# Kernel optimization log

Measured on AMD Instinct MI355X. Metric: run time of the kernel, lower is better.

Reference implementation:

```python
import jax, jax.numpy as jnp
import numpy as np

RATES = (6, 12, 18, 24)  # dilation/padding per branch


def _offset_conv(x, w, b, rate):
    # mmcv ConvModule with norm_cfg=None: conv (bias=True) + ReLU
    y = jax.lax.conv_general_dilated(
        x, w, window_strides=(1, 1),
        padding=[(rate, rate), (rate, rate)],
        rhs_dilation=(rate, rate),
        dimension_numbers=('NCHW', 'OIHW', 'NCHW'))
    return jax.nn.relu(y + b[None, :, None, None])


def _deform_conv(x, offset, w, rate):
    # DCNv1: 3x3 deformable conv, stride 1, padding=dilation=rate,
    # deformable_groups=1, no bias. Zero padding outside image (bilinear).
    B, C, H, W = x.shape
    K = 9  # 3x3 kernel taps, row-major; offset channels [2k]=dy, [2k+1]=dx
    ky = (jnp.arange(K) // 3 - 1).astype(x.dtype)
    kx = (jnp.arange(K) % 3 - 1).astype(x.dtype)
    off = offset.reshape(B, K, 2, H, W)
    gy = jnp.arange(H, dtype=x.dtype)
    gx = jnp.arange(W, dtype=x.dtype)
    # sampling coords [B,K,H,W]: p0 + dilated kernel offset + learned offset
    py = gy[None, None, :, None] + ky[None, :, None, None] * rate + off[:, :, 0]
    px = gx[None, None, None, :] + kx[None, :, None, None] * rate + off[:, :, 1]
    y0 = jnp.floor(py)
    x0 = jnp.floor(px)
    wy = (py - y0)[:, None]  # [B,1,K,H,W]
    wx = (px - x0)[:, None]
    y0i = y0.astype(jnp.int32)
    x0i = x0.astype(jnp.int32)
    xf = x.reshape(B, C, H * W)

    def gather(yi, xi):
        valid = (yi >= 0) & (yi < H) & (xi >= 0) & (xi < W)
        idx = (jnp.clip(yi, 0, H - 1) * W + jnp.clip(xi, 0, W - 1)).reshape(B, K * H * W)
        v = jnp.take_along_axis(xf, idx[:, None, :], axis=2).reshape(B, C, K, H, W)
        return v * valid[:, None].astype(x.dtype)

    samp = (gather(y0i, x0i) * (1 - wy) * (1 - wx)
            + gather(y0i, x0i + 1) * (1 - wy) * wx
            + gather(y0i + 1, x0i) * wy * (1 - wx)
            + gather(y0i + 1, x0i + 1) * wy * wx)  # [B,C,K,H,W]
    return jnp.einsum('oik,bikhw->bohw', w.reshape(w.shape[0], C, K), samp)


def setup_inputs() -> dict:
    key = jax.random.key(0)
    k1, k2, k3 = jax.random.split(key, 3)
    B, C, H, W = 2, 256, 64, 64
    Cout, R = 256, len(RATES)
    x = jax.random.normal(k1, (B, C, H, W), dtype=jnp.float32)
    dweights = jax.random.normal(k2, (R, Cout, C, 3, 3), dtype=jnp.float32) * 0.02
    oweights = jax.random.normal(k3, (R, 18, C, 3, 3), dtype=jnp.float32) * 0.01
    obias = jnp.zeros((R, 18), dtype=jnp.float32)
    return {"x": x, "dweights": dweights, "oweights": oweights, "obias": obias}


def reference(x, dweights, oweights, obias):
    R = len(RATES)
    outs = []
    for i in range(R):
        j = (i - 1) % R  # source quirk: offsets[i-1] (wraps to last for i=0)
        off = _offset_conv(x, oweights[j], obias[j], RATES[j])
        outs.append(_deform_conv(x, off, dweights[i], RATES[i]))
    return jnp.concatenate(outs, axis=1)
```

## Files before the change

### kernel.cpp

```cpp
#include <hip/hip_runtime.h>
#include <hip/hip_bf16.h>

typedef __attribute__((ext_vector_type(4))) float f32x4;
typedef __attribute__((ext_vector_type(2))) _Float16 h2;
typedef __attribute__((ext_vector_type(8))) _Float16 f16x8;

#define LGKM_BARRIER() asm volatile("s_waitcnt lgkmcnt(0)\n\ts_barrier" ::: "memory")

__global__ __launch_bounds__(256) void transpose_x_hwc_f16(const float* __restrict__ x,
                                                           unsigned short* __restrict__ x16h) {
    __shared__ float s[64][65];
    int blk = blockIdx.x;
    int b = blk >> 8, ct = (blk >> 6) & 3, pt = blk & 63;
    int c0 = ct * 64, p0 = pt * 64;
    int tid = threadIdx.x;
    int tr = tid >> 6, tc = tid & 63;
#pragma unroll
    for (int i = 0; i < 16; ++i) {
        int c = i * 4 + tr;
        s[c][tc] = x[((size_t)b * 256 + c0 + c) * 4096 + p0 + tc];
    }
    __syncthreads();
#pragma unroll
    for (int i = 0; i < 16; ++i) {
        int pp = i * 4 + tr;
        _Float16 h = (_Float16)s[tc][pp];
        x16h[((size_t)b * 4096 + p0 + pp) * 256 + c0 + tc] = *(unsigned short*)&h;
    }
}

__global__ __launch_bounds__(256) void transpose_dw_f16(const float* __restrict__ dw,
                                                        unsigned short* __restrict__ wTh) {
    int idx = blockIdx.x * 256 + threadIdx.x;
    int c = idx & 255;
    int o = (idx >> 8) & 255;
    int rest = idx >> 16;
    int k = rest % 9, i = rest / 9;
    _Float16 h = (_Float16)dw[(((i << 8) + o) * 256 + c) * 9 + k];
    wTh[idx] = *(unsigned short*)&h;
}

__global__ __launch_bounds__(256) void transpose_ow_f16(const float* __restrict__ ow,
                                                        unsigned short* __restrict__ owTh) {
    int idx = blockIdx.x * 256 + threadIdx.x;
    int c = idx & 255;
    int m = (idx >> 8) & 31;
    int rk = idx >> 13;
    int k = rk % 9, r = rk / 9;
    float v = (m < 18) ? ow[((r * 18 + m) * 256 + c) * 9 + k] : 0.f;
    _Float16 h = (_Float16)v;
    owTh[idx] = *(unsigned short*)&h;
}

__global__ __launch_bounds__(512) void offset_mfma2f(const unsigned short* __restrict__ x16h,
                                                     const unsigned short* __restrict__ owTh,
                                                     const float* __restrict__ obias,
                                                     float* __restrict__ off) {
    __shared__ short    s_a[4][32][8];
    __shared__ short    s_b[4][128][8];
    __shared__ int      s_pix[9][128];
    __shared__ unsigned s_msk[9][128];

    const int blk = blockIdx.x;
    const int r = (blk & 7) >> 1, b = blk & 1;
    const int px0 = (blk >> 3) << 7;
    const int rate = 6 * (r + 1);

    const int tid = threadIdx.x;
    const int lane = tid & 63;
    const int w = tid >> 6;
    const int kg = lane >> 4, lm = lane & 15;
    const int sg = tid >> 7, spx = tid & 127;
    const int mA = (tid & 127) >> 2, kgA = tid & 3;

    const unsigned short* xbh = x16h + (size_t)b * 1048576;
    const unsigned short* wrb = owTh + (size_t)r * 9 * 32 * 256;

    for (int e = tid; e < 1152; e += 512) {
        int k = e >> 7, pl = e & 127;
        int pg = px0 + pl;
        int yy = (pg >> 6) + (k / 3 - 1) * rate;
        int xx = (pg & 63) + (k % 3 - 1) * rate;
        bool v = ((unsigned)yy < 64u) && ((unsigned)xx < 64u);
        int cy = min(max(yy, 0), 63), cx = min(max(xx, 0), 63);
        s_pix[k][pl] = cy * 64 + cx;
        s_msk[k][pl] = v ? 0xFFFFFFFFu : 0u;
    }
    __syncthreads();

    f32x4 acc0 = (f32x4)(0.f), acc1 = (f32x4)(0.f);

    uint4 a, v;
    if (tid < 128) a = *(const uint4*)(wrb + (size_t)mA * 256 + kgA * 8);
    {
        int pix = s_pix[0][spx];
        v = *(const uint4*)(xbh + (size_t)pix * 256 + sg * 8);
    }
    unsigned m = s_msk[0][spx];

    for (int t = 0; t < 72; ++t) {
        uint4 pk = make_uint4(v.x & m, v.y & m, v.z & m, v.w & m);

        LGKM_BARRIER();
        if (tid < 128) *(uint4*)&s_a[kgA][mA][0] = a;
        *(uint4*)&s_b[sg][spx][0] = pk;
        LGKM_BARRIER();

        if (t < 71) {
            int tn = t + 1, tapn = tn >> 3, c0n = (tn & 7) << 5;
            if (tid < 128)
                a = *(const uint4*)(wrb + ((size_t)tapn * 32 + mA) * 256 + c0n + kgA * 8);
            int pix = s_pix[tapn][spx];
            m = s_msk[tapn][spx];
            v = *(const uint4*)(xbh + (size_t)pix * 256 + c0n + sg * 8);
        }

        f16x8 bf  = *(const f16x8*)&s_b[kg][w * 16 + lm][0];
        f16x8 af0 = *(const f16x8*)&s_a[kg][lm][0];
        f16x8 af1 = *(const f16x8*)&s_a[kg][16 + lm][0];
        acc0 = __builtin_amdgcn_mfma_f32_16x16x32_f16(af0, bf, acc0, 0, 0, 0);
        acc1 = __builtin_amdgcn_mfma_f32_16x16x32_f16(af1, bf, acc1, 0, 0, 0);
    }

    const float* bias = obias + r * 18;
    float* ob = off + (size_t)(r * 2 + b) * 18 * 4096;
    int px = px0 + w * 16 + lm;
#pragma unroll
    for (int reg = 0; reg < 4; ++reg) {
        int mm = kg * 4 + reg;
        ob[(size_t)mm * 4096 + px] = fmaxf(acc0[reg] + bias[mm], 0.f);
        int m1 = 16 + mm;
        if (m1 < 18)
            ob[(size_t)m1 * 4096 + px] = fmaxf(acc1[reg] + bias[m1], 0.f);
    }
}

__global__ __launch_bounds__(512, 2) void deform_mfma10(const unsigned short* __restrict__ x16h,
                                                        const unsigned short* __restrict__ wTh,
                                                        const float* __restrict__ off,
                                                        float* __restrict__ out) {
    __shared__ short  s_a[256][64];
    __shared__ short  s_b[128][64];
    __shared__ int4   s_pix[9][128];
    __shared__ float4 s_wt[9][128];

    const int blk = blockIdx.x;
    const int i = (blk & 7) >> 1, b = blk & 1;
    const int px0 = (blk >> 3) << 7;
    const int r = (i + 3) & 3;
    const int rate = 6 * (i + 1);

    const int tid = threadIdx.x;
    const int lane = tid & 63;
    const int w = tid >> 6;
    const int wo = w >> 1, wp = w & 1;
    const int kg = lane >> 4, lm = lane & 15;
    const int pxS = tid >> 2, chgS = tid & 3;
    const int oA = tid >> 3, partA = tid & 7;
    const int colA = (partA * 8) ^ ((oA & 7) * 8);

    const unsigned short* xbh = x16h + (size_t)b * 1048576;
    const float* offb = off + (size_t)(r * 2 + b) * 18 * 4096;
    const unsigned short* wib = wTh + (size_t)i * 9 * 65536;

    for (int e = tid; e < 1152; e += 512) {
        int k = e >> 7, pl = e & 127;
        int pg = px0 + pl;
        int yy = pg >> 6, xc = pg & 63;
        float dy = offb[(size_t)(2 * k) * 4096 + pg];
        float dx = offb[(size_t)(2 * k + 1) * 4096 + pg];
        float py = (float)(yy + (k / 3 - 1) * rate) + dy;
        float pxf = (float)(xc + (k % 3 - 1) * rate) + dx;
        float fy = floorf(py), fx = floorf(pxf);
        int y0 = (int)fy, x0 = (int)fx;
        float wy = py - fy, wx = pxf - fx;
        float vy0 = ((unsigned)y0 < 64u) ? 1.f : 0.f;
        float vy1 = ((unsigned)(y0 + 1) < 64u) ? 1.f : 0.f;
        float vx0 = ((unsigned)x0 < 64u) ? 1.f : 0.f;
        float vx1 = ((unsigned)(x0 + 1) < 64u) ? 1.f : 0.f;
        int cy0 = min(max(y0, 0), 63), cy1 = min(max(y0 + 1, 0), 63);
        int cx0 = min(max(x0, 0), 63), cx1 = min(max(x0 + 1, 0), 63);
        s_pix[k][pl] = make_int4(cy0 * 64 + cx0, cy0 * 64 + cx1,
                                 cy1 * 64 + cx0, cy1 * 64 + cx1);
        s_wt[k][pl] = make_float4(vy0 * vx0 * (1.f - wy) * (1.f - wx),
                                  vy0 * vx1 * (1.f - wy) * wx,
                                  vy1 * vx0 * wy * (1.f - wx),
                                  vy1 * vx1 * wy * wx);
    }
    __syncthreads();

    f32x4 acc[4][4];
#pragma unroll
    for (int mi = 0; mi < 4; ++mi)
#pragma unroll
        for (int ni = 0; ni < 4; ++ni) acc[mi][ni] = (f32x4)(0.f);

    uint4 a0, a1, a2, a3;
    uint4 u0, u1, u2, u3, w0, w1, w2, w3;
    {
        const unsigned short* wrow = wib + partA * 8;
        a0 = *(const uint4*)(wrow + (size_t)(oA      ) * 256);
        a1 = *(const uint4*)(wrow + (size_t)(oA +  64) * 256);
        a2 = *(const uint4*)(wrow + (size_t)(oA + 128) * 256);
        a3 = *(const uint4*)(wrow + (size_t)(oA + 192) * 256);
        int4 p = s_pix[0][pxS];
        const unsigned short* xch = xbh + chgS * 8;
        u0 = *(const uint4*)(xch + ((size_t)p.x << 8));
        u1 = *(const uint4*)(xch + ((size_t)p.y << 8));
        u2 = *(const uint4*)(xch + ((size_t)p.z << 8));
        u3 = *(const uint4*)(xch + ((size_t)p.w << 8));
        w0 = *(const uint4*)(xch + ((size_t)p.x << 8) + 32);
        w1 = *(const uint4*)(xch + ((size_t)p.y << 8) + 32);
        w2 = *(const uint4*)(xch + ((size_t)p.z << 8) + 32);
        w3 = *(const uint4*)(xch + ((size_t)p.w << 8) + 32);
    }

    for (int t = 0; t < 36; ++t) {
        const int tap = t >> 2;

        uint4 pkA, pkB;
        {
            float4 qwf = s_wt[tap][pxS];
            h2 qx = (h2)((_Float16)qwf.x), qy = (h2)((_Float16)qwf.y);
            h2 qz = (h2)((_Float16)qwf.z), qv = (h2)((_Float16)qwf.w);
            h2 r0 = (*(h2*)&u0.x) * qx + (*(h2*)&u1.x) * qy + (*(h2*)&u2.x) * qz + (*(h2*)&u3.x) * qv;
            h2 r1 = (*(h2*)&u0.y) * qx + (*(h2*)&u1.y) * qy + (*(h2*)&u2.y) * qz + (*(h2*)&u3.y) * qv;
            h2 r2 = (*(h2*)&u0.z) * qx + (*(h2*)&u1.z) * qy + (*(h2*)&u2.z) * qz + (*(h2*)&u3.z) * qv;
            h2 r3 = (*(h2*)&u0.w) * qx + (*(h2*)&u1.w) * qy + (*(h2*)&u2.w) * qz + (*(h2*)&u3.w) * qv;
            pkA = make_uint4(*(unsigned*)&r0, *(unsigned*)&r1, *(unsigned*)&r2, *(unsigned*)&r3);
            h2 s0 = (*(h2*)&w0.x) * qx + (*(h2*)&w1.x) * qy + (*(h2*)&w2.x) * qz + (*(h2*)&w3.x) * qv;
            h2 s1 = (*(h2*)&w0.y) * qx + (*(h2*)&w1.y) * qy + (*(h2*)&w2.y) * qz + (*(h2*)&w3.y) * qv;
            h2 s2 = (*(h2*)&w0.z) * qx + (*(h2*)&w1.z) * qy + (*(h2*)&w2.z) * qz + (*(h2*)&w3.z) * qv;
            h2 s3 = (*(h2*)&w0.w) * qx + (*(h2*)&w1.w) * qy + (*(h2*)&w2.w) * qz + (*(h2*)&w3.w) * qv;
            pkB = make_uint4(*(unsigned*)&s0, *(unsigned*)&s1, *(unsigned*)&s2, *(unsigned*)&s3);
        }

        LGKM_BARRIER();
        *(uint4*)&s_a[oA      ][colA] = a0;
        *(uint4*)&s_a[oA +  64][colA] = a1;
        *(uint4*)&s_a[oA + 128][colA] = a2;
        *(uint4*)&s_a[oA + 192][colA] = a3;
        *(uint4*)&s_b[pxS][(chgS ^ (pxS & 7)) * 8]       = pkA;
        *(uint4*)&s_b[pxS][((chgS + 4) ^ (pxS & 7)) * 8] = pkB;
        LGKM_BARRIER();

        if (t < 35) {
            int tn = t + 1, tapn = tn >> 2, c0n = (tn & 3) << 6;
            const unsigned short* wrow = wib + (size_t)tapn * 65536 + c0n + partA * 8;
            a0 = *(const uint4*)(wrow + (size_t)(oA      ) * 256);
            a1 = *(const uint4*)(wrow + (size_t)(oA +  64) * 256);
            a2 = *(const uint4*)(wrow + (size_t)(oA + 128) * 256);
            a3 = *(const uint4*)(wrow + (size_t)(oA + 192) * 256);
            int4 p = s_pix[tapn][pxS];
            const unsigned short* xch = xbh + c0n + chgS * 8;
            u0 = *(const uint4*)(xch + ((size_t)p.x << 8));
            u1 = *(const uint4*)(xch + ((size_t)p.y << 8));
            u2 = *(const uint4*)(xch + ((size_t)p.z << 8));
            u3 = *(const uint4*)(xch + ((size_t)p.w << 8));
            w0 = *(const uint4*)(xch + ((size_t)p.x << 8) + 32);
            w1 = *(const uint4*)(xch + ((size_t)p.y << 8) + 32);
            w2 = *(const uint4*)(xch + ((size_t)p.z << 8) + 32);
            w3 = *(const uint4*)(xch + ((size_t)p.w << 8) + 32);
        }

#pragma unroll
        for (int kf = 0; kf < 2; ++kf) {
            int oct = kf * 4 + kg;
            int col = (oct ^ (lm & 7)) * 8;
            f16x8 bf0 = *(const f16x8*)&s_b[wp * 64 + lm][col];
            f16x8 bf1 = *(const f16x8*)&s_b[wp * 64 + 16 + lm][col];
            f16x8 bf2 = *(const f16x8*)&s_b[wp * 64 + 32 + lm][col];
            f16x8 bf3 = *(const f16x8*)&s_b[wp * 64 + 48 + lm][col];
#pragma unroll
            for (int mi = 0; mi < 4; ++mi) {
                f16x8 af = *(const f16x8*)&s_a[wo * 64 + mi * 16 + lm][col];
                acc[mi][0] = __builtin_amdgcn_mfma_f32_16x16x32_f16(af, bf0, acc[mi][0], 0, 0, 0);
                acc[mi][1] = __builtin_amdgcn_mfma_f32_16x16x32_f16(af, bf1, acc[mi][1], 0, 0, 0);
                acc[mi][2] = __builtin_amdgcn_mfma_f32_16x16x32_f16(af, bf2, acc[mi][2], 0, 0, 0);
                acc[mi][3] = __builtin_amdgcn_mfma_f32_16x16x32_f16(af, bf3, acc[mi][3], 0, 0, 0);
            }
        }
    }

    float* ob = out + ((size_t)b * 1024 + i * 256) * 4096;
#pragma unroll
    for (int mi = 0; mi < 4; ++mi) {
        int o = wo * 64 + mi * 16 + kg * 4;
#pragma unroll
        for (int ni = 0; ni < 4; ++ni) {
            int pg = px0 + wp * 64 + ni * 16 + lm;
#pragma unroll
            for (int reg = 0; reg < 4; ++reg)
                ob[(size_t)(o + reg) * 4096 + pg] = acc[mi][ni][reg];
        }
    }
}

extern "C" void kernel_launch(void* const* d_in, const int* in_sizes, int n_in,
                              void* d_out, int out_size, void* d_ws, size_t ws_size,
                              hipStream_t stream) {
    const float* x  = (const float*)d_in[0];
    const float* dw = (const float*)d_in[1];
    const float* ow = (const float*)d_in[2];
    const float* ob = (const float*)d_in[3];
    float* out = (float*)d_out;

    float* ws  = (float*)d_ws;
    float* off = ws;
    unsigned short* wTh  = (unsigned short*)(ws + 589824);
    unsigned short* owTh = wTh + 2359296;
    unsigned short* x16h = (unsigned short*)(ws + 1916928);

    transpose_x_hwc_f16<<<512, 256, 0, stream>>>(x, x16h);
    transpose_dw_f16<<<9216, 256, 0, stream>>>(dw, wTh);
    transpose_ow_f16<<<1152, 256, 0, stream>>>(ow, owTh);
    offset_mfma2f<<<256, 512, 0, stream>>>(x16h, owTh, ob, off);
    deform_mfma10<<<256, 512, 0, stream>>>(x16h, wTh, off, out);
}
```

Before: 110.6 us.

## Double K-chunk per barrier in offset and deform kernels; tile weight transpose via LDS

Both MFMA kernels now stage twice as many input channels into LDS per iteration, which halves the number of barrier-synchronised loop steps (72→36 for the offset conv, 36→18 for the deform conv). The deform kernel keeps two sets of bilinear corner loads in flight per phase. Separately, the deform weight transpose now reads each output row contiguously into shared memory instead of doing strided scalar gathers. The cost is larger LDS buffers and many more live registers, which may lower occupancy under the 512-thread, 2-block launch bound or cause spills.

After: 106.7 us. 3.5% less time.

```diff
diff --git a/kernel.cpp b/kernel.cpp
--- a/kernel.cpp
+++ b/kernel.cpp
@@ -6,6 +6,15 @@
 typedef __attribute__((ext_vector_type(8))) _Float16 f16x8;
 
 #define LGKM_BARRIER() asm volatile("s_waitcnt lgkmcnt(0)\n\ts_barrier" ::: "memory")
+
+__device__ __forceinline__ uint4 lerp4(uint4 c0, uint4 c1, uint4 c2, uint4 c3,
+                                       h2 qx, h2 qy, h2 qz, h2 qv) {
+    h2 r0 = (*(h2*)&c0.x) * qx + (*(h2*)&c1.x) * qy + (*(h2*)&c2.x) * qz + (*(h2*)&c3.x) * qv;
+    h2 r1 = (*(h2*)&c0.y) * qx + (*(h2*)&c1.y) * qy + (*(h2*)&c2.y) * qz + (*(h2*)&c3.y) * qv;
+    h2 r2 = (*(h2*)&c0.z) * qx + (*(h2*)&c1.z) * qy + (*(h2*)&c2.z) * qz + (*(h2*)&c3.z) * qv;
+    h2 r3 = (*(h2*)&c0.w) * qx + (*(h2*)&c1.w) * qy + (*(h2*)&c2.w) * qz + (*(h2*)&c3.w) * qv;
+    return make_uint4(*(unsigned*)&r0, *(unsigned*)&r1, *(unsigned*)&r2, *(unsigned*)&r3);
+}
 
 __global__ __launch_bounds__(256) void transpose_x_hwc_f16(const float* __restrict__ x,
                                                            unsigned short* __restrict__ x16h) {
@@ -31,13 +40,20 @@
 
 __global__ __launch_bounds__(256) void transpose_dw_f16(const float* __restrict__ dw,
                                                         unsigned short* __restrict__ wTh) {
-    int idx = blockIdx.x * 256 + threadIdx.x;
-    int c = idx & 255;
-    int o = (idx >> 8) & 255;
-    int rest = idx >> 16;
-    int k = rest % 9, i = rest / 9;
-    _Float16 h = (_Float16)dw[(((i << 8) + o) * 256 + c) * 9 + k];
-    wTh[idx] = *(unsigned short*)&h;
+    __shared__ float s[2304];
+    int blk = blockIdx.x;
+    int i = blk >> 8, o = blk & 255;
+    const float* src = dw + (size_t)(i * 256 + o) * 2304;
+    int tid = threadIdx.x;
+#pragma unroll
+    for (int e = tid; e < 576; e += 256)
+        *(float4*)&s[e * 4] = *(const float4*)&src[e * 4];
+    __syncthreads();
+#pragma unroll
+    for (int k = 0; k < 9; ++k) {
+        _Float16 h = (_Float16)s[tid * 9 + k];
+        wTh[(((size_t)i * 9 + k) * 256 + o) * 256 + tid] = *(unsigned short*)&h;
+    }
 }
 
 __global__ __launch_bounds__(256) void transpose_ow_f16(const float* __restrict__ ow,
@@ -52,12 +68,12 @@
     owTh[idx] = *(unsigned short*)&h;
 }
 
-__global__ __launch_bounds__(512) void offset_mfma2f(const unsigned short* __restrict__ x16h,
+__global__ __launch_bounds__(512) void offset_mfma3f(const unsigned short* __restrict__ x16h,
                                                      const unsigned short* __restrict__ owTh,
                                                      const float* __restrict__ obias,
                                                      float* __restrict__ off) {
-    __shared__ short    s_a[4][32][8];
-    __shared__ short    s_b[4][128][8];
+    __shared__ short    s_a[8][32][8];
+    __shared__ short    s_b[8][128][8];
     __shared__ int      s_pix[9][128];
     __shared__ unsigned s_msk[9][128];
 
@@ -90,36 +106,52 @@
 
     f32x4 acc0 = (f32x4)(0.f), acc1 = (f32x4)(0.f);
 
-    uint4 a, v;
-    if (tid < 128) a = *(const uint4*)(wrb + (size_t)mA * 256 + kgA * 8);
+    uint4 a_lo, a_hi, v_lo, v_hi;
+    if (tid < 128) {
+        a_lo = *(const uint4*)(wrb + (size_t)mA * 256 + kgA * 8);
+        a_hi = *(const uint4*)(wrb + (size_t)mA * 256 + 32 + kgA * 8);
+    }
     {
         int pix = s_pix[0][spx];
-        v = *(const uint4*)(xbh + (size_t)pix * 256 + sg * 8);
+        v_lo = *(const uint4*)(xbh + (size_t)pix * 256 + sg * 8);
+        v_hi = *(const uint4*)(xbh + (size_t)pix * 256 + 32 + sg * 8);
     }
     unsigned m = s_msk[0][spx];
 
-    for (int t = 0; t < 72; ++t) {
-        uint4 pk = make_uint4(v.x & m, v.y & m, v.z & m, v.w & m);
+    for (int t = 0; t < 36; ++t) {
+        uint4 pkl = make_uint4(v_lo.x & m, v_lo.y & m, v_lo.z & m, v_lo.w & m);
+        uint4 pkh = make_uint4(v_hi.x & m, v_hi.y & m, v_hi.z & m, v_hi.w & m);
 
         LGKM_BARRIER();
-        if (tid < 128) *(uint4*)&s_a[kgA][mA][0] = a;
-        *(uint4*)&s_b[sg][spx][0] = pk;
+        if (tid < 128) {
+            *(uint4*)&s_a[kgA][mA][0]     = a_lo;
+            *(uint4*)&s_a[kgA + 4][mA][0] = a_hi;
+        }
+        *(uint4*)&s_b[sg][spx][0]     = pkl;
+        *(uint4*)&s_b[sg + 4][spx][0] = pkh;
         LGKM_BARRIER();
 
-        if (t < 71) {
-            int tn = t + 1, tapn = tn >> 3, c0n = (tn & 7) << 5;
-            if (tid < 128)
-                a = *(const uint4*)(wrb + ((size_t)tapn * 32 + mA) * 256 + c0n + kgA * 8);
+        if (t < 35) {
+            int tn = t + 1, tapn = tn >> 2, c0n = (tn & 3) << 6;
+            if (tid < 128) {
+                a_lo = *(const uint4*)(wrb + ((size_t)tapn * 32 + mA) * 256 + c0n + kgA * 8);
+                a_hi = *(const uint4*)(wrb + ((size_t)tapn * 32 + mA) * 256 + c0n + 32 + kgA * 8);
+            }
             int pix = s_pix[tapn][spx];
             m = s_msk[tapn][spx];
-            v = *(const uint4*)(xbh + (size_t)pix * 256 + c0n + sg * 8);
-        }
-
-        f16x8 bf  = *(const f16x8*)&s_b[kg][w * 16 + lm][0];
-        f16x8 af0 = *(const f16x8*)&s_a[kg][lm][0];
-        f16x8 af1 = *(const f16x8*)&s_a[kg][16 + lm][0];
-        acc0 = __builtin_amdgcn_mfma_f32_16x16x32_f16(af0, bf, acc0, 0, 0, 0);
-        acc1 = __builtin_amdgcn_mfma_f32_16x16x32_f16(af1, bf, acc1, 0, 0, 0);
+            v_lo = *(const uint4*)(xbh + (size_t)pix * 256 + c0n + sg * 8);
+            v_hi = *(const uint4*)(xbh + (size_t)pix * 256 + c0n + 32 + sg * 8);
+        }
+
+#pragma unroll
+        for (int kf = 0; kf < 2; ++kf) {
+            int oct = kf * 4 + kg;
+            f16x8 bf  = *(const f16x8*)&s_b[oct][w * 16 + lm][0];
+            f16x8 af0 = *(const f16x8*)&s_a[oct][lm][0];
+            f16x8 af1 = *(const f16x8*)&s_a[oct][16 + lm][0];
+            acc0 = __builtin_amdgcn_mfma_f32_16x16x32_f16(af0, bf, acc0, 0, 0, 0);
+            acc1 = __builtin_amdgcn_mfma_f32_16x16x32_f16(af1, bf, acc1, 0, 0, 0);
+        }
     }
 
     const float* bias = obias + r * 18;
@@ -135,12 +167,12 @@
     }
 }
 
-__global__ __launch_bounds__(512, 2) void deform_mfma10(const unsigned short* __restrict__ x16h,
+__global__ __launch_bounds__(512, 2) void deform_mfma11(const unsigned short* __restrict__ x16h,
                                                         const unsigned short* __restrict__ wTh,
                                                         const float* __restrict__ off,
                                                         float* __restrict__ out) {
-    __shared__ short  s_a[256][64];
-    __shared__ short  s_b[128][64];
+    __shared__ short  s_a[256][128];
+    __shared__ short  s_b[128][128];
     __shared__ int4   s_pix[9][128];
     __shared__ float4 s_wt[9][128];
 
@@ -157,7 +189,7 @@
     const int kg = lane >> 4, lm = lane & 15;
     const int pxS = tid >> 2, chgS = tid & 3;
     const int oA = tid >> 3, partA = tid & 7;
-    const int colA = (partA * 8) ^ ((oA & 7) * 8);
+    const int colA = (partA ^ (oA & 7)) * 8;
 
     const unsigned short* xbh = x16h + (size_t)b * 1048576;
     const float* offb = off + (size_t)(r * 2 + b) * 18 * 4096;
@@ -195,89 +227,129 @@
 #pragma unroll
         for (int ni = 0; ni < 4; ++ni) acc[mi][ni] = (f32x4)(0.f);
 
-    uint4 a0, a1, a2, a3;
-    uint4 u0, u1, u2, u3, w0, w1, w2, w3;
+    uint4 aA0, aA1, aA2, aA3, aB0, aB1, aB2, aB3;
+    uint4 c00, c01, c02, c03, c10, c11, c12, c13;
+    uint4 d00, d01, d02, d03, d10, d11, d12, d13;
+
     {
-        const unsigned short* wrow = wib + partA * 8;
-        a0 = *(const uint4*)(wrow + (size_t)(oA      ) * 256);
-        a1 = *(const uint4*)(wrow + (size_t)(oA +  64) * 256);
-        a2 = *(const uint4*)(wrow + (size_t)(oA + 128) * 256);
-        a3 = *(const uint4*)(wrow + (size_t)(oA + 192) * 256);
+        const unsigned short* wr0 = wib + partA * 8;
+        aA0 = *(const uint4*)(wr0 + (size_t)(oA      ) * 256);
+        aA1 = *(const uint4*)(wr0 + (size_t)(oA +  64) * 256);
+        aA2 = *(const uint4*)(wr0 + (size_t)(oA + 128) * 256);
+        aA3 = *(const uint4*)(wr0 + (size_t)(oA + 192) * 256);
+        const unsigned short* wr1 = wr0 + 64;
+        aB0 = *(const uint4*)(wr1 + (size_t)(oA      ) * 256);
+        aB1 = *(const uint4*)(wr1 + (size_t)(oA +  64) * 256);
+        aB2 = *(const uint4*)(wr1 + (size_t)(oA + 128) * 256);
+        aB3 = *(const uint4*)(wr1 + (size_t)(oA + 192) * 256);
         int4 p = s_pix[0][pxS];
-        const unsigned short* xch = xbh + chgS * 8;
-        u0 = *(const uint4*)(xch + ((size_t)p.x << 8));
-        u1 = *(const uint4*)(xch + ((size_t)p.y << 8));
-        u2 = *(const uint4*)(xch + ((size_t)p.z << 8));
-        u3 = *(const uint4*)(xch + ((size_t)p.w << 8));
-        w0 = *(const uint4*)(xch + ((size_t)p.x << 8) + 32);
-        w1 = *(const uint4*)(xch + ((size_t)p.y << 8) + 32);
-        w2 = *(const uint4*)(xch + ((size_t)p.z << 8) + 32);
-        w3 = *(const uint4*)(xch + ((size_t)p.w << 8) + 32);
-    }
-
-    for (int t = 0; t < 36; ++t) {
-        const int tap = t >> 2;
-
-        uint4 pkA, pkB;
+        const unsigned short* x0p = xbh + chgS * 8;
+        c00 = *(const uint4*)(x0p + ((size_t)p.x << 8));
+        c01 = *(const uint4*)(x0p + ((size_t)p.y << 8));
+        c02 = *(const uint4*)(x0p + ((size_t)p.z << 8));
+        c03 = *(const uint4*)(x0p + ((size_t)p.w << 8));
+        c10 = *(const uint4*)(x0p + ((size_t)p.x << 8) + 32);
+        c11 = *(const uint4*)(x0p + ((size_t)p.y << 8) + 32);
+        c12 = *(const uint4*)(x0p + ((size_t)p.z << 8) + 32);
+        c13 = *(const uint4*)(x0p + ((size_t)p.w << 8) + 32);
+        const unsigned short* x1p = x0p + 64;
+        d00 = *(const uint4*)(x1p + ((size_t)p.x << 8));
+        d01 = *(const uint4*)(x1p + ((size_t)p.y << 8));
+        d02 = *(const uint4*)(x1p + ((size_t)p.z << 8));
+        d03 = *(const uint4*)(x1p + ((size_t)p.w << 8));
+        d10 = *(const uint4*)(x1p + ((size_t)p.x << 8) + 32);
+        d11 = *(const uint4*)(x1p + ((size_t)p.y << 8) + 32);
+        d12 = *(const uint4*)(x1p + ((size_t)p.z << 8) + 32);
+        d13 = *(const uint4*)(x1p + ((size_t)p.w << 8) + 32);
+    }
+
+    for (int ph = 0; ph < 18; ++ph) {
+        const int s0 = 2 * ph, s1 = 2 * ph + 1;
+        const int tap0 = s0 >> 2, tap1 = s1 >> 2;
+
+        uint4 pkA0, pkA1, pkB0, pkB1;
         {
-            float4 qwf = s_wt[tap][pxS];
-            h2 qx = (h2)((_Float16)qwf.x), qy = (h2)((_Float16)qwf.y);
-            h2 qz = (h2)((_Float16)qwf.z), qv = (h2)((_Float16)qwf.w);
-            h2 r0 = (*(h2*)&u0.x) * qx + (*(h2*)&u1.x) * qy + (*(h2*)&u2.x) * qz + (*(h2*)&u3.x) * qv;
-            h2 r1 = (*(h2*)&u0.y) * qx + (*(h2*)&u1.y) * qy + (*(h2*)&u2.y) * qz + (*(h2*)&u3.y) * qv;
-            h2 r2 = (*(h2*)&u0.z) * qx + (*(h2*)&u1.z) * qy + (*(h2*)&u2.z) * qz + (*(h2*)&u3.z) * qv;
-            h2 r3 = (*(h2*)&u0.w) * qx + (*(h2*)&u1.w) * qy + (*(h2*)&u2.w) * qz + (*(h2*)&u3.w) * qv;
-            pkA = make_uint4(*(unsigned*)&r0, *(unsigned*)&r1, *(unsigned*)&r2, *(unsigned*)&r3);
-            h2 s0 = (*(h2*)&w0.x) * qx + (*(h2*)&w1.x) * qy + (*(h2*)&w2.x) * qz + (*(h2*)&w3.x) * qv;
-            h2 s1 = (*(h2*)&w0.y) * qx + (*(h2*)&w1.y) * qy + (*(h2*)&w2.y) * qz + (*(h2*)&w3.y) * qv;
-            h2 s2 = (*(h2*)&w0.z) * qx + (*(h2*)&w1.z) * qy + (*(h2*)&w2.z) * qz + (*(h2*)&w3.z) * qv;
-            h2 s3 = (*(h2*)&w0.w) * qx + (*(h2*)&w1.w) * qy + (*(h2*)&w2.w) * qz + (*(h2*)&w3.w) * qv;
-            pkB = make_uint4(*(unsigned*)&s0, *(unsigned*)&s1, *(unsigned*)&s2, *(unsigned*)&s3);
+            float4 q0 = s_wt[tap0][pxS];
+            h2 qx = (h2)((_Float16)q0.x), qy = (h2)((_Float16)q0.y);
+            h2 qz = (h2)((_Float16)q0.z), qv = (h2)((_Float16)q0.w);
+            pkA0 = lerp4(c00, c01, c02, c03, qx, qy, qz, qv);
+            pkA1 = lerp4(c10, c11, c12, c13, qx, qy, qz, qv);
+            float4 q1 = s_wt[tap1][pxS];
+            h2 rx = (h2)((_Float16)q1.x), ry = (h2)((_Float16)q1.y);
+            h2 rz = (h2)((_Float16)q1.z), rv = (h2)((_Float16)q1.w);
+            pkB0 = lerp4(d00, d01, d02, d03, rx, ry, rz, rv);
+            pkB1 = lerp4(d10, d11, d12, d13, rx, ry, rz, rv);
         }
 
         LGKM_BARRIER();
-        *(uint4*)&s_a[oA      ][colA] = a0;
-        *(uint4*)&s_a[oA +  64][colA] = a1;
-        *(uint4*)&s_a[oA + 128][colA] = a2;
-        *(uint4*)&s_a[oA + 192][colA] = a3;
-        *(uint4*)&s_b[pxS][(chgS ^ (pxS & 7)) * 8]       = pkA;
-        *(uint4*)&s_b[pxS][((chgS + 4) ^ (pxS & 7)) * 8] = pkB;
+        *(uint4*)&s_a[oA      ][colA]      = aA0;
+        *(uint4*)&s_a[oA +  64][colA]      = aA1;
+        *(uint4*)&s_a[oA + 128][colA]      = aA2;
+        *(uint4*)&s_a[oA + 192][colA]      = aA3;
+        *(uint4*)&s_a[oA      ][64 + colA] = aB0;
+        *(uint4*)&s_a[oA +  64][64 + colA] = aB1;
+        *(uint4*)&s_a[oA + 128][64 + colA] = aB2;
+        *(uint4*)&s_a[oA + 192][64 + colA] = aB3;
+        *(uint4*)&s_b[pxS][(chgS ^ (pxS & 7)) * 8]            = pkA0;
+        *(uint4*)&s_b[pxS][((chgS + 4) ^ (pxS & 7)) * 8]      = pkA1;
+        *(uint4*)&s_b[pxS][64 + (chgS ^ (pxS & 7)) * 8]       = pkB0;
+        *(uint4*)&s_b[pxS][64 + ((chgS + 4) ^ (pxS & 7)) * 8] = pkB1;
         LGKM_BARRIER();
 
-        if (t < 35) {
-            int tn = t + 1, tapn = tn >> 2, c0n = (tn & 3) << 6;
-            const unsigned short* wrow = wib + (size_t)tapn * 65536 + c0n + partA * 8;
-            a0 = *(const uint4*)(wrow + (size_t)(oA      ) * 256);
-            a1 = *(const uint4*)(wrow + (size_t)(oA +  64) * 256);
-            a2 = *(const uint4*)(wrow + (size_t)(oA + 128) * 256);
-            a3 = *(const uint4*)(wrow + (size_t)(oA + 192) * 256);
-            int4 p = s_pix[tapn][pxS];
-            const unsigned short* xch = xbh + c0n + chgS * 8;
-            u0 = *(const uint4*)(xch + ((size_t)p.x << 8));
-            u1 = *(const uint4*)(xch + ((size_t)p.y << 8));
-            u2 = *(const uint4*)(xch + ((size_t)p.z << 8));
-            u3 = *(const uint4*)(xch + ((size_t)p.w << 8));
-            w0 = *(const uint4*)(xch + ((size_t)p.x << 8) + 32);
-            w1 = *(const uint4*)(xch + ((size_t)p.y << 8) + 32);
-            w2 = *(const uint4*)(xch + ((size_t)p.z << 8) + 32);
-            w3 = *(const uint4*)(xch + ((size_t)p.w << 8) + 32);
-        }
-
-#pragma unroll
-        for (int kf = 0; kf < 2; ++kf) {
-            int oct = kf * 4 + kg;
-            int col = (oct ^ (lm & 7)) * 8;
-            f16x8 bf0 = *(const f16x8*)&s_b[wp * 64 + lm][col];
-            f16x8 bf1 = *(const f16x8*)&s_b[wp * 64 + 16 + lm][col];
-            f16x8 bf2 = *(const f16x8*)&s_b[wp * 64 + 32 + lm][col];
-            f16x8 bf3 = *(const f16x8*)&s_b[wp * 64 + 48 + lm][col];
-#pragma unroll
-            for (int mi = 0; mi < 4; ++mi) {
-                f16x8 af = *(const f16x8*)&s_a[wo * 64 + mi * 16 + lm][col];
-                acc[mi][0] = __builtin_amdgcn_mfma_f32_16x16x32_f16(af, bf0, acc[mi][0], 0, 0, 0);
-                acc[mi][1] = __builtin_amdgcn_mfma_f32_16x16x32_f16(af, bf1, acc[mi][1], 0, 0, 0);
-                acc[mi][2] = __builtin_amdgcn_mfma_f32_16x16x32_f16(af, bf2, acc[mi][2], 0, 0, 0);
-                acc[mi][3] = __builtin_amdgcn_mfma_f32_16x16x32_f16(af, bf3, acc[mi][3], 0, 0, 0);
+        if (ph < 17) {
+            int n0 = s0 + 2, n1 = s0 + 3;
+            int tA = n0 >> 2, cA = (n0 & 3) << 6;
+            int tB = n1 >> 2, cB = (n1 & 3) << 6;
+            const unsigned short* wr0 = wib + (size_t)tA * 65536 + cA + partA * 8;
+            aA0 = *(const uint4*)(wr0 + (size_t)(oA      ) * 256);
+            aA1 = *(const uint4*)(wr0 + (size_t)(oA +  64) * 256);
+            aA2 = *(const uint4*)(wr0 + (size_t)(oA + 128) * 256);
+            aA3 = *(const uint4*)(wr0 + (size_t)(oA + 192) * 256);
+            const unsigned short* wr1 = wib + (size_t)tB * 65536 + cB + partA * 8;
+            aB0 = *(const uint4*)(wr1 + (size_t)(oA      ) * 256);
+            aB1 = *(const uint4*)(wr1 + (size_t)(oA +  64) * 256);
+            aB2 = *(const uint4*)(wr1 + (size_t)(oA + 128) * 256);
+            aB3 = *(const uint4*)(wr1 + (size_t)(oA + 192) * 256);
+            int4 p0 = s_pix[tA][pxS];
+            const unsigned short* x0p = xbh + cA + chgS * 8;
+            c00 = *(const uint4*)(x0p + ((size_t)p0.x << 8));
+            c01 = *(const uint4*)(x0p + ((size_t)p0.y << 8));
+            c02 = *(const uint4*)(x0p + ((size_t)p0.z << 8));
+            c03 = *(const uint4*)(x0p + ((size_t)p0.w << 8));
+            c10 = *(const uint4*)(x0p + ((size_t)p0.x << 8) + 32);
+            c11 = *(const uint4*)(x0p + ((size_t)p0.y << 8) + 32);
+            c12 = *(const uint4*)(x0p + ((size_t)p0.z << 8) + 32);
+            c13 = *(const uint4*)(x0p + ((size_t)p0.w << 8) + 32);
+            int4 p1 = s_pix[tB][pxS];
+            const unsigned short* x1p = xbh + cB + chgS * 8;
+            d00 = *(const uint4*)(x1p + ((size_t)p1.x << 8));
+            d01 = *(const uint4*)(x1p + ((size_t)p1.y << 8));
+            d02 = *(const uint4*)(x1p + ((size_t)p1.z << 8));
+            d03 = *(const uint4*)(x1p + ((size_t)p1.w << 8));
+            d10 = *(const uint4*)(x1p + ((size_t)p1.x << 8) + 32);
+            d11 = *(const uint4*)(x1p + ((size_t)p1.y << 8) + 32);
+            d12 = *(const uint4*)(x1p + ((size_t)p1.z << 8) + 32);
+            d13 = *(const uint4*)(x1p + ((size_t)p1.w << 8) + 32);
+        }
+
+#pragma unroll
+        for (int sub = 0; sub < 2; ++sub) {
+#pragma unroll
+            for (int kf = 0; kf < 2; ++kf) {
+                int oct = kf * 4 + kg;
+                int col = sub * 64 + (oct ^ (lm & 7)) * 8;
+                f16x8 bf0 = *(const f16x8*)&s_b[wp * 64 + lm][col];
+                f16x8 bf1 = *(const f16x8*)&s_b[wp * 64 + 16 + lm][col];
+                f16x8 bf2 = *(const f16x8*)&s_b[wp * 64 + 32 + lm][col];
+                f16x8 bf3 = *(const f16x8*)&s_b[wp * 64 + 48 + lm][col];
+#pragma unroll
+                for (int mi = 0; mi < 4; ++mi) {
+                    f16x8 af = *(const f16x8*)&s_a[wo * 64 + mi * 16 + lm][col];
+                    acc[mi][0] = __builtin_amdgcn_mfma_f32_16x16x32_f16(af, bf0, acc[mi][0], 0, 0, 0);
+                    acc[mi][1] = __builtin_amdgcn_mfma_f32_16x16x32_f16(af, bf1, acc[mi][1], 0, 0, 0);
+                    acc[mi][2] = __builtin_amdgcn_mfma_f32_16x16x32_f16(af, bf2, acc[mi][2], 0, 0, 0);
+                    acc[mi][3] = __builtin_amdgcn_mfma_f32_16x16x32_f16(af, bf3, acc[mi][3], 0, 0, 0);
+                }
             }
         }
     }
@@ -312,8 +384,8 @@
     unsigned short* x16h = (unsigned short*)(ws + 1916928);
 
     transpose_x_hwc_f16<<<512, 256, 0, stream>>>(x, x16h);
-    transpose_dw_f16<<<9216, 256, 0, stream>>>(dw, wTh);
+    transpose_dw_f16<<<1024, 256, 0, stream>>>(dw, wTh);
     transpose_ow_f16<<<1152, 256, 0, stream>>>(ow, owTh);
-    offset_mfma2f<<<256, 512, 0, stream>>>(x16h, owTh, ob, off);
-    deform_mfma10<<<256, 512, 0, stream>>>(x16h, wTh, off, out);
-}
+    offset_mfma3f<<<256, 512, 0, stream>>>(x16h, owTh, ob, off);
+    deform_mfma11<<<256, 512, 0, stream>>>(x16h, wTh, off, out);
+}
```
